# Kernel optimization log

Measured on AMD Instinct MI355X. Metric: run time of the kernel, lower is better.

The kernel has to match this reference:

```python
import jax, jax.numpy as jnp
import numpy as np

EPSILON = 8.0        # Gibbs kernel temperature (JCPOTConfig.epsilon)
NUM_INNER_ITER = 10  # Sinkhorn u/v fixed-point iterations
STAB = 1e-8          # denominator stabilizer, matches torch code


def _cost_matrix(s, t):
    # Euclidean pairwise distance, same math as torch.norm(s[:,None]-t[None,:], dim=2)
    # computed without materializing the [n_s, n_t, d] tensor.
    sq = jnp.sum(s * s, axis=1)[:, None] + jnp.sum(t * t, axis=1)[None, :] - 2.0 * (s @ t.T)
    return jnp.sqrt(jnp.maximum(sq, 0.0))


def setup_inputs() -> dict:
    key = jax.random.key(0)
    k1, k2 = jax.random.split(key)
    return {
        "source_features": jax.random.normal(k1, (4096, 512), dtype=jnp.float32),
        "target_features": jax.random.normal(k2, (4096, 512), dtype=jnp.float32),
    }


def reference(source_features, target_features):
    n_s = source_features.shape[0]
    n_t = target_features.shape[0]
    C = _cost_matrix(source_features, target_features)   # [n_s, n_t]
    K = jnp.exp(-C / EPSILON)                             # Gibbs kernel

    # uniform marginals (JCPOT passes uniform weights; Sinkhorn renormalizes -> same)
    a = jnp.full((n_s, 1), 1.0 / n_s, dtype=C.dtype)
    b = jnp.full((n_t, 1), 1.0 / n_t, dtype=C.dtype)

    def body(carry, _):
        u, v = carry
        u = a / (K @ v + STAB)
        v = b / (K.T @ u + STAB)
        return (u, v), None

    u0 = jnp.ones((n_s, 1), dtype=C.dtype)
    v0 = jnp.ones((n_t, 1), dtype=C.dtype)
    (u, v), _ = jax.lax.scan(body, (u0, v0), None, length=NUM_INNER_ITER)

    coupling = u * K * v.T                                # [n_s, n_t]
    ot_loss = jnp.sum(coupling * C) / (n_s * n_t)         # reduction='mean'
    # returns same contents as the torch dict: ot_loss, coupling, cost_matrix
    return ot_loss, coupling, C
```

## Files before the change

### kernel.cpp

```cpp
#include <hip/hip_runtime.h>
#include <math.h>


#define N_S 4096
#define N_T 4096
#define DIM 512
#define STAB 1e-8f

typedef _Float16 f16x2 __attribute__((ext_vector_type(2)));
typedef _Float16 f16x4 __attribute__((ext_vector_type(4)));
typedef _Float16 f16x8 __attribute__((ext_vector_type(8)));
typedef float f32x4v __attribute__((ext_vector_type(4)));

__global__ __launch_bounds__(256) void k_norms(const float4* __restrict__ S4,
                                               const float4* __restrict__ T4,
                                               float* __restrict__ ns, float* __restrict__ nt) {
    int t = threadIdx.x;
    int lane = t & 63, wave = t >> 6;
    int wid = blockIdx.x * 4 + wave;
    const float4* src; float* dst; int row;
    if (wid < N_S) { src = S4; dst = ns; row = wid; }
    else           { src = T4; dst = nt; row = wid - N_S; }
    float acc = 0.f;
#pragma unroll
    for (int c = 0; c < 2; ++c) {
        float4 x = src[row * 128 + c * 64 + lane];
        acc += x.x*x.x + x.y*x.y + x.z*x.z + x.w*x.w;
    }
#pragma unroll
    for (int m = 32; m; m >>= 1) acc += __shfl_xor(acc, m);
    if (lane == 0) dst[row] = acc;
}

__global__ void k_init(float* v, float* vacc, double* lossd) {
    int g = blockIdx.x * 256 + threadIdx.x;
    if (g < N_T) { v[g] = 1.0f; vacc[g] = 0.0f; }
    if (g == 0) *lossd = 0.0;
}

template<int MODE>
__global__ __launch_bounds__(256) void k_gemm(const float* __restrict__ S, const float* __restrict__ T,
                                              const float* __restrict__ ns, const float* __restrict__ nt,
                                              float* __restrict__ outK, _Float16* __restrict__ outKh,
                                              float* __restrict__ outC) {
    __shared__ _Float16 As[128 * 40];
    __shared__ _Float16 Bs[128 * 40];
    int t = threadIdx.x;
    int lane = t & 63, wave = t >> 6;
    int wr = wave >> 1, wc = wave & 1;
    int brow = blockIdx.x * 128, bcol = blockIdx.y * 128;

    f32x4v acc[4][4] = {};

    for (int kt = 0; kt < DIM; kt += 32) {
        __syncthreads();
#pragma unroll
        for (int w = 0; w < 4; ++w) {
            int e = w * 1024 + t * 4;
            int row = e >> 5, col = e & 31;
            float4 a = *(const float4*)(S + (size_t)(brow + row) * DIM + kt + col);
            f16x4 ah = { (_Float16)a.x, (_Float16)a.y, (_Float16)a.z, (_Float16)a.w };
            *(f16x4*)(&As[row * 40 + col]) = ah;
            float4 b = *(const float4*)(T + (size_t)(bcol + row) * DIM + kt + col);
            f16x4 bh = { (_Float16)b.x, (_Float16)b.y, (_Float16)b.z, (_Float16)b.w };
            *(f16x4*)(&Bs[row * 40 + col]) = bh;
        }
        __syncthreads();

        f16x8 af[4], bf[4];
#pragma unroll
        for (int m = 0; m < 4; ++m)
            af[m] = *(const f16x8*)(&As[(wr * 64 + m * 16 + (lane & 15)) * 40 + (lane >> 4) * 8]);
#pragma unroll
        for (int n = 0; n < 4; ++n)
            bf[n] = *(const f16x8*)(&Bs[(wc * 64 + n * 16 + (lane & 15)) * 40 + (lane >> 4) * 8]);
#pragma unroll
        for (int m = 0; m < 4; ++m)
#pragma unroll
            for (int n = 0; n < 4; ++n)
                acc[m][n] = __builtin_amdgcn_mfma_f32_16x16x32_f16(af[m], bf[n], acc[m][n], 0, 0, 0);
    }

#pragma unroll
    for (int m = 0; m < 4; ++m) {
#pragma unroll
        for (int n = 0; n < 4; ++n) {
#pragma unroll
            for (int r = 0; r < 4; ++r) {
                int i = brow + wr * 64 + m * 16 + (lane >> 4) * 4 + r;
                int j = bcol + wc * 64 + n * 16 + (lane & 15);
                float dot = acc[m][n][r];
                float sq = ns[i] + nt[j] - 2.0f * dot;
                float c = sqrtf(fmaxf(sq, 0.0f));
                float k = __expf(-c * 0.125f);
                size_t idx = (size_t)i * N_T + j;
                outC[idx] = c;
                if constexpr (MODE == 0) outK[idx] = k;
                else                     outKh[idx] = (_Float16)k;
            }
        }
    }
}

__global__ __launch_bounds__(256) void k_sink(const _Float16* __restrict__ Kh,
                                              const float* __restrict__ v,
                                              float* __restrict__ u_out,
                                              float* __restrict__ part) {
    __shared__ _Float16 rows[4][4096];
    __shared__ float u_s[4];
    int t = threadIdx.x, lane = t & 63, w = t >> 6;
    float2 acc[8];
#pragma unroll
    for (int s = 0; s < 8; ++s) acc[s] = make_float2(0.f, 0.f);

    for (int c = 0; c < 2; ++c) {
        if (c) __syncthreads();
        int row = blockIdx.x * 8 + c * 4 + w;
        const _Float16* Kr = Kh + (size_t)row * N_T;
        float dot = 0.f;
#pragma unroll
        for (int it = 0; it < 8; ++it) {
            int j0 = it * 512 + lane * 8;
            f16x8 kv = *(const f16x8*)(Kr + j0);
            float4 v0 = *(const float4*)(v + j0);
            float4 v1 = *(const float4*)(v + j0 + 4);
            *(f16x8*)(&rows[w][j0]) = kv;
            dot += (float)kv[0]*v0.x + (float)kv[1]*v0.y + (float)kv[2]*v0.z + (float)kv[3]*v0.w
                 + (float)kv[4]*v1.x + (float)kv[5]*v1.y + (float)kv[6]*v1.z + (float)kv[7]*v1.w;
        }
#pragma unroll
        for (int m = 32; m; m >>= 1) dot += __shfl_xor(dot, m);
        if (lane == 0) {
            float uv = (1.0f / N_S) / (dot + STAB);
            u_s[w] = uv;
            u_out[row] = uv;
        }
        __syncthreads();
#pragma unroll
        for (int s = 0; s < 8; ++s) {
            int jj = t * 2 + s * 512;
#pragma unroll
            for (int r = 0; r < 4; ++r) {
                f16x2 kk = *(const f16x2*)(&rows[r][jj]);
                float uu = u_s[r];
                acc[s].x += uu * (float)kk[0];
                acc[s].y += uu * (float)kk[1];
            }
        }
    }
    float* pb = part + (size_t)blockIdx.x * N_T;
#pragma unroll
    for (int s = 0; s < 8; ++s)
        *(float2*)(pb + t * 2 + s * 512) = acc[s];
}

__global__ __launch_bounds__(256) void k_vfin2(const float* __restrict__ part, float* __restrict__ v) {
    __shared__ float sums[256];
    int t = threadIdx.x;
    int jl = t & 15, c = t >> 4;
    int j = blockIdx.x * 16 + jl;
    float acc = 0.f;
#pragma unroll 8
    for (int k = 0; k < 32; ++k)
        acc += part[(size_t)(c * 32 + k) * N_T + j];
    sums[t] = acc;
    __syncthreads();
    if (t < 16) {
        float s = 0.f;
#pragma unroll
        for (int c2 = 0; c2 < 16; ++c2) s += sums[c2 * 16 + t];
        v[blockIdx.x * 16 + t] = (1.0f / N_T) / (s + STAB);
    }
}

__global__ __launch_bounds__(256) void k_final2(const _Float16* __restrict__ Kh, const float* __restrict__ Cd,
                                                const float* __restrict__ u, const float* __restrict__ v,
                                                float* __restrict__ W, double* __restrict__ lossd) {
    int t = threadIdx.x, row = blockIdx.x;
    float ui = u[row];
    float lacc = 0.f;
    const _Float16* Kr = Kh + (size_t)row * N_T;
    const float* Cr = Cd + (size_t)row * N_T;
    float* Wr = W + (size_t)row * N_T;
#pragma unroll
    for (int cc = 0; cc < 4; ++cc) {
        int j = (cc * 256 + t) * 4;
        f16x4 kk = *(const f16x4*)(Kr + j);
        float4 c4 = *(const float4*)(Cr + j);
        float4 v4 = *(const float4*)(v + j);
        float4 w4;
        w4.x = ui * (float)kk[0] * v4.x;
        w4.y = ui * (float)kk[1] * v4.y;
        w4.z = ui * (float)kk[2] * v4.z;
        w4.w = ui * (float)kk[3] * v4.w;
        *(float4*)(Wr + j) = w4;
        lacc += w4.x*c4.x + w4.y*c4.y + w4.z*c4.z + w4.w*c4.w;
    }
#pragma unroll
    for (int m = 32; m; m >>= 1) lacc += __shfl_xor(lacc, m);
    __shared__ float wsum[4];
    int lane = t & 63, wave = t >> 6;
    if (lane == 0) wsum[wave] = lacc;
    __syncthreads();
    if (t == 0) atomicAdd(lossd, (double)(wsum[0] + wsum[1] + wsum[2] + wsum[3]));
}

__global__ void k_loss(const double* __restrict__ lossd, float* __restrict__ out0) {
    *out0 = (float)(*lossd / ((double)N_S * (double)N_T));
}

__global__ __launch_bounds__(256) void k_rowmv(const float* __restrict__ Kd,
                                               const float* __restrict__ v, float* __restrict__ u) {
    __shared__ float vl[4096];
    int t = threadIdx.x;
#pragma unroll
    for (int c = 0; c < 16; ++c) vl[c * 256 + t] = v[c * 256 + t];
    __syncthreads();
    int lane = t & 63, wave = t >> 6;
    int row = blockIdx.x * 4 + wave;
    const float* Kr = Kd + (size_t)row * N_T;
    float dot = 0.f;
#pragma unroll 8
    for (int c = 0; c < 64; ++c) {
        int j = c * 64 + lane;
        dot += Kr[j] * vl[j];
    }
#pragma unroll
    for (int m = 32; m; m >>= 1) dot += __shfl_xor(dot, m);
    if (lane == 0) u[row] = (1.0f / N_S) / (dot + STAB);
}

__global__ __launch_bounds__(256) void k_colmv(const float* __restrict__ Kd,
                                               const float* __restrict__ u, float* __restrict__ vacc) {
    __shared__ float ul[64];
    int t = threadIdx.x;
    int rc = blockIdx.y;
    if (t < 64) ul[t] = u[rc * 64 + t];
    __syncthreads();
    int j = blockIdx.x * 256 + t;
    const float* Kp = Kd + (size_t)(rc * 64) * N_T + j;
    float acc = 0.f;
#pragma unroll 8
    for (int r = 0; r < 64; ++r) acc += Kp[(size_t)r * N_T] * ul[r];
    atomicAdd(&vacc[j], acc);
}

__global__ void k_vfin(float* v, float* vacc) {
    int j = blockIdx.x * 256 + threadIdx.x;
    v[j] = (1.0f / N_T) / (vacc[j] + STAB);
    vacc[j] = 0.f;
}

__global__ __launch_bounds__(256) void k_final(float* __restrict__ Kd, const float* __restrict__ Cd,
                                               const float* __restrict__ u, const float* __restrict__ v,
                                               double* __restrict__ lossd) {
    int t = threadIdx.x;
    int row = blockIdx.x;
    float ui = u[row];
    float lacc = 0.f;
#pragma unroll 4
    for (int c = 0; c < 16; ++c) {
        int j = c * 256 + t;
        size_t idx = (size_t)row * N_T + j;
        float w = ui * Kd[idx] * v[j];
        Kd[idx] = w;
        lacc += w * Cd[idx];
    }
#pragma unroll
    for (int m = 32; m; m >>= 1) lacc += __shfl_xor(lacc, m);
    __shared__ float wsum[4];
    int lane = t & 63, wave = t >> 6;
    if (lane == 0) wsum[wave] = lacc;
    __syncthreads();
    if (t == 0) atomicAdd(lossd, (double)(wsum[0] + wsum[1] + wsum[2] + wsum[3]));
}

extern "C" void kernel_launch(void* const* d_in, const int* in_sizes, int n_in,
                              void* d_out, int out_size, void* d_ws, size_t ws_size,
                              hipStream_t stream) {
    const float* S = (const float*)d_in[0];
    const float* T = (const float*)d_in[1];
    float* out = (float*)d_out;
    float* outCoup = out + 1;
    float* outC = out + 1 + (size_t)N_S * N_T;

    const size_t KH_BYTES = (size_t)N_S * N_T * 2;
    const size_t PART_BYTES = (size_t)512 * N_T * 4;
    const size_t need = KH_BYTES + PART_BYTES + 4 * 16384 + 16;

    if (ws_size >= need) {
        _Float16* kh = (_Float16*)d_ws;
        float* part = (float*)((char*)d_ws + KH_BYTES);
        float* ns = (float*)((char*)d_ws + KH_BYTES + PART_BYTES);
        float* nt = ns + 4096;
        float* u  = nt + 4096;
        float* v  = u + 4096;
        double* lossd = (double*)(v + 4096);

        k_norms<<<2048, 256, 0, stream>>>((const float4*)S, (const float4*)T, ns, nt);
        k_init<<<16, 256, 0, stream>>>(v, part, lossd);
        k_gemm<1><<<dim3(32, 32), 256, 0, stream>>>(S, T, ns, nt, nullptr, kh, outC);
        for (int it = 0; it < 10; ++it) {
            k_sink<<<512, 256, 0, stream>>>(kh, v, u, part);
            k_vfin2<<<256, 256, 0, stream>>>(part, v);
        }
        k_final2<<<4096, 256, 0, stream>>>(kh, outC, u, v, outCoup, lossd);
        k_loss<<<1, 1, 0, stream>>>(lossd, out);
    } else {
        float* outK = outCoup;
        float* ws   = (float*)d_ws;
        float* ns   = ws;
        float* nt   = ws + 4096;
        float* u    = ws + 8192;
        float* v    = ws + 12288;
        float* vacc = ws + 16384;
        double* lossd = (double*)(ws + 20480);

        k_norms<<<2048, 256, 0, stream>>>((const float4*)S, (const float4*)T, ns, nt);
        k_init<<<16, 256, 0, stream>>>(v, vacc, lossd);
        k_gemm<0><<<dim3(32, 32), 256, 0, stream>>>(S, T, ns, nt, outK, nullptr, outC);
        for (int it = 0; it < 10; ++it) {
            k_rowmv<<<1024, 256, 0, stream>>>(outK, v, u);
            k_colmv<<<dim3(16, 64), 256, 0, stream>>>(outK, u, vacc);
            k_vfin<<<16, 256, 0, stream>>>(v, vacc);
        }
        k_final<<<4096, 256, 0, stream>>>(outK, outC, u, v, lossd);
        k_loss<<<1, 1, 0, stream>>>(lossd, out);
    }
}
```

Measured before the change: 389.8 us.

## Fuse Sinkhorn iterations into one cooperative kernel holding K in LDS

The GEMM now writes only the cost matrix. A single cooperative kernel with 256 blocks recomputes the fp16 Gibbs kernel from C, with each block keeping its 16 rows in 128KB of shared memory. It then runs all 10 u/v iterations with grid.sync between the row and column phases, and finishes with the coupling and the loss, which uses the log of K instead of rereading C. This is meant to remove the repeated global reads of the fp16 K matrix and about 20 kernel launches. In exchange it depends on co-residency of 256 blocks and on grid-wide barriers, and keeps the old multi-kernel path as a fallback if the cooperative launch fails.

```diff
diff --git a/kernel.cpp b/kernel.cpp
--- a/kernel.cpp
+++ b/kernel.cpp
@@ -1,5 +1,8 @@
 #include <hip/hip_runtime.h>
+#include <hip/hip_cooperative_groups.h>
 #include <math.h>
+
+namespace cg = cooperative_groups;
 
 
 #define N_S 4096
@@ -11,6 +14,8 @@
 typedef _Float16 f16x4 __attribute__((ext_vector_type(4)));
 typedef _Float16 f16x8 __attribute__((ext_vector_type(8)));
 typedef float f32x4v __attribute__((ext_vector_type(4)));
+
+#define COOP_SMEM (131072 + 64 + 512 + 2048)
 
 __global__ __launch_bounds__(256) void k_norms(const float4* __restrict__ S4,
                                                const float4* __restrict__ T4,
@@ -92,14 +97,156 @@
                 float dot = acc[m][n][r];
                 float sq = ns[i] + nt[j] - 2.0f * dot;
                 float c = sqrtf(fmaxf(sq, 0.0f));
-                float k = __expf(-c * 0.125f);
                 size_t idx = (size_t)i * N_T + j;
                 outC[idx] = c;
-                if constexpr (MODE == 0) outK[idx] = k;
-                else                     outKh[idx] = (_Float16)k;
+                if constexpr (MODE == 0) outK[idx] = __expf(-c * 0.125f);
+                if constexpr (MODE == 1) outKh[idx] = (_Float16)__expf(-c * 0.125f);
             }
         }
     }
+}
+
+__global__ __launch_bounds__(512, 1) void k_coop(const float* __restrict__ Cd,
+                                                 float* __restrict__ W,
+                                                 float* __restrict__ part,
+                                                 float* __restrict__ v,
+                                                 double* __restrict__ lossd) {
+    cg::grid_group grid = cg::this_grid();
+    extern __shared__ char smem[];
+    _Float16* Ksh = (_Float16*)smem;
+    float* u_s  = (float*)(smem + 131072);
+    float* wred = (float*)(smem + 131072 + 64);
+    float* cred = (float*)(smem + 131072 + 64 + 512);
+
+    const int t = threadIdx.x;
+    const int lane = t & 63, wave = t >> 6;
+    const int b = blockIdx.x;
+    const int base = t * 8;
+
+    const float* Crow = Cd + (size_t)b * (16 * 4096);
+
+#pragma unroll
+    for (int i = 0; i < 16; ++i) {
+        const float* cp = Crow + i * 4096 + base;
+        float4 c0 = *(const float4*)cp;
+        float4 c1 = *(const float4*)(cp + 4);
+        f16x8 h;
+        h[0] = (_Float16)__expf(c0.x * -0.125f);
+        h[1] = (_Float16)__expf(c0.y * -0.125f);
+        h[2] = (_Float16)__expf(c0.z * -0.125f);
+        h[3] = (_Float16)__expf(c0.w * -0.125f);
+        h[4] = (_Float16)__expf(c1.x * -0.125f);
+        h[5] = (_Float16)__expf(c1.y * -0.125f);
+        h[6] = (_Float16)__expf(c1.z * -0.125f);
+        h[7] = (_Float16)__expf(c1.w * -0.125f);
+        *(f16x8*)(Ksh + i * 4096 + base) = h;
+    }
+    __syncthreads();
+
+    for (int it = 0; it < 10; ++it) {
+        float4 v0 = *(const float4*)(v + base);
+        float4 v1 = *(const float4*)(v + base + 4);
+        float vf[8] = {v0.x, v0.y, v0.z, v0.w, v1.x, v1.y, v1.z, v1.w};
+#pragma unroll
+        for (int i = 0; i < 16; ++i) {
+            f16x8 k8 = *(const f16x8*)(Ksh + i * 4096 + base);
+            float p = 0.f;
+#pragma unroll
+            for (int c = 0; c < 8; ++c) p += (float)k8[c] * vf[c];
+#pragma unroll
+            for (int m = 32; m; m >>= 1) p += __shfl_xor(p, m);
+            if (lane == 0) wred[wave * 16 + i] = p;
+        }
+        __syncthreads();
+        if (t < 16) {
+            float s = 0.f;
+#pragma unroll
+            for (int w = 0; w < 8; ++w) s += wred[w * 16 + t];
+            u_s[t] = (1.0f / N_S) / (s + STAB);
+        }
+        __syncthreads();
+        float acc[8] = {0.f,0.f,0.f,0.f,0.f,0.f,0.f,0.f};
+#pragma unroll
+        for (int i = 0; i < 16; ++i) {
+            f16x8 k8 = *(const f16x8*)(Ksh + i * 4096 + base);
+            float ui = u_s[i];
+#pragma unroll
+            for (int c = 0; c < 8; ++c) acc[c] += ui * (float)k8[c];
+        }
+        float* pp = part + (size_t)b * 4096 + base;
+        *(float4*)pp       = make_float4(acc[0], acc[1], acc[2], acc[3]);
+        *(float4*)(pp + 4) = make_float4(acc[4], acc[5], acc[6], acc[7]);
+        grid.sync();
+        {
+            int c = t & 15, p0 = t >> 4;
+            int j = b * 16 + c;
+            float s = 0.f;
+#pragma unroll
+            for (int k = 0; k < 8; ++k)
+                s += part[(size_t)(p0 * 8 + k) * 4096 + j];
+            cred[p0 * 16 + c] = s;
+        }
+        __syncthreads();
+        if (t < 16) {
+            float s2 = 0.f;
+#pragma unroll
+            for (int k = 0; k < 32; ++k) s2 += cred[k * 16 + t];
+            v[b * 16 + t] = (1.0f / N_T) / (s2 + STAB);
+        }
+        grid.sync();
+    }
+
+    float4 v0 = *(const float4*)(v + base);
+    float4 v1 = *(const float4*)(v + base + 4);
+    float vf[8] = {v0.x, v0.y, v0.z, v0.w, v1.x, v1.y, v1.z, v1.w};
+    float lacc = 0.f;
+    const float NEG8LN2 = -5.5451774444795623f;
+#pragma unroll
+    for (int i = 0; i < 16; ++i) {
+        f16x8 k8 = *(const f16x8*)(Ksh + i * 4096 + base);
+        float ui = u_s[i];
+        float w[8];
+#pragma unroll
+        for (int c = 0; c < 8; ++c) {
+            float kf = (float)k8[c];
+            float wc = ui * kf * vf[c];
+            w[c] = wc;
+            lacc += wc * (NEG8LN2 * __log2f(kf));
+        }
+        float* wp = W + (size_t)(b * 16 + i) * 4096 + base;
+        *(float4*)wp       = make_float4(w[0], w[1], w[2], w[3]);
+        *(float4*)(wp + 4) = make_float4(w[4], w[5], w[6], w[7]);
+    }
+#pragma unroll
+    for (int m = 32; m; m >>= 1) lacc += __shfl_xor(lacc, m);
+    if (lane == 0) wred[wave] = lacc;
+    __syncthreads();
+    if (t == 0) {
+        float s = 0.f;
+#pragma unroll
+        for (int w = 0; w < 8; ++w) s += wred[w];
+        atomicAdd(lossd, (double)s);
+    }
+}
+
+__global__ void k_loss(const double* __restrict__ lossd, float* __restrict__ out0) {
+    *out0 = (float)(*lossd / ((double)N_S * (double)N_T));
+}
+
+__global__ __launch_bounds__(256) void k_kh(const float* __restrict__ Cd, _Float16* __restrict__ Kh) {
+    size_t i = ((size_t)blockIdx.x * 256 + threadIdx.x) * 8;
+    float4 c0 = *(const float4*)(Cd + i);
+    float4 c1 = *(const float4*)(Cd + i + 4);
+    f16x8 h;
+    h[0] = (_Float16)__expf(c0.x * -0.125f);
+    h[1] = (_Float16)__expf(c0.y * -0.125f);
+    h[2] = (_Float16)__expf(c0.z * -0.125f);
+    h[3] = (_Float16)__expf(c0.w * -0.125f);
+    h[4] = (_Float16)__expf(c1.x * -0.125f);
+    h[5] = (_Float16)__expf(c1.y * -0.125f);
+    h[6] = (_Float16)__expf(c1.z * -0.125f);
+    h[7] = (_Float16)__expf(c1.w * -0.125f);
+    *(f16x8*)(Kh + i) = h;
 }
 
 __global__ __launch_bounds__(256) void k_sink(const _Float16* __restrict__ Kh,
@@ -205,10 +352,6 @@
     if (t == 0) atomicAdd(lossd, (double)(wsum[0] + wsum[1] + wsum[2] + wsum[3]));
 }
 
-__global__ void k_loss(const double* __restrict__ lossd, float* __restrict__ out0) {
-    *out0 = (float)(*lossd / ((double)N_S * (double)N_T));
-}
-
 __global__ __launch_bounds__(256) void k_rowmv(const float* __restrict__ Kd,
                                                const float* __restrict__ v, float* __restrict__ u) {
     __shared__ float vl[4096];
@@ -284,28 +427,42 @@
     float* outCoup = out + 1;
     float* outC = out + 1 + (size_t)N_S * N_T;
 
-    const size_t KH_BYTES = (size_t)N_S * N_T * 2;
-    const size_t PART_BYTES = (size_t)512 * N_T * 4;
-    const size_t need = KH_BYTES + PART_BYTES + 4 * 16384 + 16;
+    const size_t MB = 1024 * 1024;
+    const size_t need = 40 * MB + 64 * 1024 + 16;
 
     if (ws_size >= need) {
-        _Float16* kh = (_Float16*)d_ws;
-        float* part = (float*)((char*)d_ws + KH_BYTES);
-        float* ns = (float*)((char*)d_ws + KH_BYTES + PART_BYTES);
+        char* wsb = (char*)d_ws;
+        float* partC   = (float*)wsb;
+        _Float16* kh   = (_Float16*)wsb;
+        float* part8   = (float*)(wsb + 32 * MB);
+        float* ns = (float*)(wsb + 40 * MB);
         float* nt = ns + 4096;
         float* u  = nt + 4096;
         float* v  = u + 4096;
         double* lossd = (double*)(v + 4096);
 
         k_norms<<<2048, 256, 0, stream>>>((const float4*)S, (const float4*)T, ns, nt);
-        k_init<<<16, 256, 0, stream>>>(v, part, lossd);
-        k_gemm<1><<<dim3(32, 32), 256, 0, stream>>>(S, T, ns, nt, nullptr, kh, outC);
-        for (int it = 0; it < 10; ++it) {
-            k_sink<<<512, 256, 0, stream>>>(kh, v, u, part);
-            k_vfin2<<<256, 256, 0, stream>>>(part, v);
-        }
-        k_final2<<<4096, 256, 0, stream>>>(kh, outC, u, v, outCoup, lossd);
-        k_loss<<<1, 1, 0, stream>>>(lossd, out);
+        k_init<<<16, 256, 0, stream>>>(v, partC, lossd);
+        k_gemm<2><<<dim3(32, 32), 256, 0, stream>>>(S, T, ns, nt, nullptr, nullptr, outC);
+
+        (void)hipFuncSetAttribute((const void*)k_coop,
+                                  hipFuncAttributeMaxDynamicSharedMemorySize, COOP_SMEM);
+        const float* CdArg = outC; float* WArg = outCoup; float* partArg = partC;
+        float* vArg = v; double* ldArg = lossd;
+        void* args[5] = { &CdArg, &WArg, &partArg, &vArg, &ldArg };
+        hipError_t ce = hipLaunchCooperativeKernel((const void*)k_coop, dim3(256), dim3(512),
+                                                   args, (unsigned)COOP_SMEM, stream);
+        if (ce == hipSuccess) {
+            k_loss<<<1, 1, 0, stream>>>(lossd, out);
+        } else {
+            k_kh<<<8192, 256, 0, stream>>>(outC, kh);
+            for (int it = 0; it < 10; ++it) {
+                k_sink<<<512, 256, 0, stream>>>(kh, v, u, part8);
+                k_vfin2<<<256, 256, 0, stream>>>(part8, v);
+            }
+            k_final2<<<4096, 256, 0, stream>>>(kh, outC, u, v, outCoup, lossd);
+            k_loss<<<1, 1, 0, stream>>>(lossd, out);
+        }
     } else {
         float* outK = outCoup;
         float* ws   = (float*)d_ws;
```

Result: slower. 910.1 us (+133.5%).
